# Performance work log

Measured on AMD Instinct MI355X. Metric: run time of the kernel, lower is better.

## Reference

```python
import jax, jax.numpy as jnp
import numpy as np

B, S, D = 16, 2000, 512          # batch, seq_len, input_dim
G, K = 2, 320                    # num_groups, num_vars
CV = 256                         # codevector_dim
d = CV // G                      # per-group codevector dim
TAU = 2.0                        # gumbel-softmax temperature (module default)
EPS = 1e-7


def setup_inputs() -> dict:
    key = jax.random.key(0)
    k0, k1, k2, k3, k4 = jax.random.split(key, 5)
    hidden_states = jax.random.normal(k0, (B, S, D), jnp.float32)
    mask_time_indices = jax.random.randint(k1, (B, S), 0, 2) > 0
    W = jax.random.normal(k2, (G * K, D), jnp.float32) * 0.02  # weight_proj
    b = jnp.zeros((G * K,), jnp.float32)
    codevectors = jax.random.uniform(k3, (1, G * K, d), jnp.float32)  # uniform_ init
    u = jax.random.uniform(k4, (B * S * G, K), jnp.float32, minval=1e-6, maxval=1.0 - 1e-6)
    gumbel = -jnp.log(-jnp.log(u))  # standard Gumbel(0,1) noise
    return dict(hidden_states=hidden_states, mask_time_indices=mask_time_indices,
                W=W, b=b, codevectors=codevectors, gumbel=gumbel)


def _compute_perplexity(probs, mask):
    # probs: (B*S, G, K); mask: (B, S) bool
    mask_f = mask.reshape(-1).astype(probs.dtype)[:, None, None]
    marginal = (probs * mask_f).sum(0) / mask_f.sum()          # (G, K)
    return jnp.exp(-jnp.sum(marginal * jnp.log(marginal + EPS), axis=-1)).sum()


def reference(hidden_states, mask_time_indices, W, b, codevectors, gumbel):
    # weight projection: (B, S, G*K)
    logits = jnp.einsum('bsd,vd->bsv', hidden_states, W) + b
    logits = logits.reshape(B * S * G, K)

    # hard gumbel-softmax (training path), straight-through estimator
    y_soft = jax.nn.softmax((logits + gumbel) / TAU, axis=-1)
    idx = jnp.argmax(y_soft, axis=-1)
    y_hard = jax.nn.one_hot(idx, K, dtype=y_soft.dtype)
    codevector_probs = y_hard + y_soft - jax.lax.stop_gradient(y_soft)

    # perplexity from the soft (non-gumbel, non-tempered) distribution
    soft_dist = jax.nn.softmax(logits.reshape(B * S, G, K), axis=-1)
    perplexity = _compute_perplexity(soft_dist, mask_time_indices)

    # weighted sum of codevectors per group; einsum avoids the (B*S, G*K, d) blowup
    cv = codevectors.reshape(G, K, d)
    out = jnp.einsum('ngk,gkd->ngd', codevector_probs.reshape(B * S, G, K), cv)
    out = out.reshape(B, S, G * d)  # (B, S, codevector_dim)
    return out, perplexity
```

## Files before the change

### kernel.cpp

```cpp
#include <hip/hip_runtime.h>

#define NB    16
#define NS    2000
#define ND    512
#define NG    2
#define NK    320
#define NV    640
#define NDCV  128
#define NTOK  32000
#define TAUF  2.0f
#define EPSF  1e-7f

#define TPB      16
#define NTHREADS 640
#define TIE_THR  2.5e-3f

using half8   = __attribute__((ext_vector_type(8))) _Float16;
using half4   = __attribute__((ext_vector_type(4))) _Float16;
using float4v = __attribute__((ext_vector_type(4))) float;

__device__ inline half8 cvt8hi(float4 p0, float4 p1) {
    half8 a;
    a[0] = (_Float16)p0.x; a[1] = (_Float16)p0.y;
    a[2] = (_Float16)p0.z; a[3] = (_Float16)p0.w;
    a[4] = (_Float16)p1.x; a[5] = (_Float16)p1.y;
    a[6] = (_Float16)p1.z; a[7] = (_Float16)p1.w;
    return a;
}

__device__ inline half4 cvt4hi(float4 p) {
    half4 a;
    a[0] = (_Float16)p.x; a[1] = (_Float16)p.y;
    a[2] = (_Float16)p.z; a[3] = (_Float16)p.w;
    return a;
}

__device__ inline bool beats(float za, int ka, float zb, int kb) {
    return (za > zb) || (za == zb && ka < kb);
}

__global__ void k_wsplit(const float* __restrict__ W, half8* __restrict__ W1p) {
    int t = blockIdx.x * 256 + threadIdx.x;
    if (t >= NV * (ND / 8)) return;
    int v  = t % NV;
    int kc = t / NV;
    const float* src = W + (size_t)v * ND + kc * 8;
    float4 p0 = *(const float4*)src;
    float4 p1 = *(const float4*)(src + 4);
    W1p[t] = cvt8hi(p0, p1);
}

#define AROWB 128
__global__ __launch_bounds__(1024, 4) void k_gemm(
    const float* __restrict__ hidden,
    const half8* __restrict__ W1p,
    const float* __restrict__ bvec,
    float* __restrict__ logits)
{
    __shared__ __align__(16) char Abuf[2][64 * AROWB];

    const int t    = threadIdx.x;
    const int lane = t & 63;
    const int w    = t >> 6;
    const int wn   = w & 7;
    const int wm   = w >> 3;
    const int l15  = lane & 15;
    const int l4   = lane >> 4;
    const int n0b  = blockIdx.x * 64;

    const int sm  = t >> 4;
    const int sk4 = t & 15;
    const float* hrow = hidden + (size_t)(n0b + sm) * ND + sk4 * 4;
    const int wbyte = sm * AROWB + ((((sk4 >> 1) ^ (sm & 7)) << 4) | ((sk4 & 1) << 3));

    float4v acc[2][5];
    #pragma unroll
    for (int mt = 0; mt < 2; ++mt)
        #pragma unroll
        for (int nt = 0; nt < 5; ++nt) acc[mt][nt] = (float4v)0.0f;

    {
        float4 p = *(const float4*)(hrow);
        *(half4*)(&Abuf[0][wbyte]) = cvt4hi(p);
    }
    __syncthreads();

    const half8* bbase = W1p + (size_t)l4 * NV + wn * 80 + l15;

    for (int c = 0; c < 8; ++c) {
        float4 p;
        if (c < 7) p = *(const float4*)(hrow + (c + 1) * 64);

        const char* base = Abuf[c & 1];
        #pragma unroll
        for (int ks = 0; ks < 2; ++ks) {
            half8 b[5];
            #pragma unroll
            for (int nt = 0; nt < 5; ++nt)
                b[nt] = bbase[(size_t)(c * 8 + ks * 4) * NV + nt * 16];

            const int xr = ((ks * 4 + l4) ^ (l15 & 7)) << 4;
            half8 fa[2];
            #pragma unroll
            for (int mt = 0; mt < 2; ++mt)
                fa[mt] = *(const half8*)(base + (wm * 32 + mt * 16 + l15) * AROWB + xr);

            #pragma unroll
            for (int nt = 0; nt < 5; ++nt)
                #pragma unroll
                for (int mt = 0; mt < 2; ++mt)
                    acc[mt][nt] = __builtin_amdgcn_mfma_f32_16x16x32_f16(fa[mt], b[nt], acc[mt][nt], 0, 0, 0);
        }

        if (c < 7)
            *(half4*)(&Abuf[(c + 1) & 1][wbyte]) = cvt4hi(p);
        __syncthreads();
    }

    #pragma unroll
    for (int nt = 0; nt < 5; ++nt) {
        const int col = wn * 80 + nt * 16 + l15;
        const float bb = bvec[col];
        #pragma unroll
        for (int mt = 0; mt < 2; ++mt) {
            #pragma unroll
            for (int r = 0; r < 4; ++r) {
                const int row = n0b + wm * 32 + mt * 16 + l4 * 4 + r;
                logits[(size_t)row * NV + col] = acc[mt][nt][r] + bb;
            }
        }
    }
}

#define EPI_BLOCKS  1024
#define EPI_THREADS 256
#define EPI_SLOTS   (EPI_BLOCKS * (EPI_THREADS / 16))
#define NPAIRS      (NTOK * NG)

__global__ __launch_bounds__(EPI_THREADS) void k_epi(
    const float* __restrict__ logits,
    const float* __restrict__ gumbel,
    const int*   __restrict__ mask,
    const float* __restrict__ hidden,
    const float* __restrict__ W,
    const float* __restrict__ bvec,
    const float* __restrict__ codevec,
    float* __restrict__ out,
    float* __restrict__ marginal)
{
    __shared__ float marg[NV];
    const int t     = threadIdx.x;
    const int lane  = t & 63;
    const int q     = lane >> 4;
    const int ql    = lane & 15;
    const int wslot = blockIdx.x * (EPI_THREADS / 16) + (t >> 4);
    const int g     = wslot & 1;

    for (int i = t; i < NV; i += EPI_THREADS) marg[i] = 0.f;
    __syncthreads();

    float mreg[5][4] = {};

    int pair = wslot;
    float4 cl[5], cg[5];
    {
        const float* lrow = logits + (size_t)(pair >> 1) * NV + g * NK;
        const float* grow = gumbel + (size_t)pair * NK;
        #pragma unroll
        for (int j = 0; j < 5; ++j) {
            cl[j] = *(const float4*)(lrow + 64 * j + 4 * ql);
            cg[j] = *(const float4*)(grow + 64 * j + 4 * ql);
        }
    }

    while (true) {
        const int npair = pair + EPI_SLOTS;
        const bool nvalid = npair < NPAIRS;
        float4 nl[5], ng[5];
        if (nvalid) {
            const float* lrow = logits + (size_t)(npair >> 1) * NV + g * NK;
            const float* grow = gumbel + (size_t)npair * NK;
            #pragma unroll
            for (int j = 0; j < 5; ++j) {
                nl[j] = *(const float4*)(lrow + 64 * j + 4 * ql);
                ng[j] = *(const float4*)(grow + 64 * j + 4 * ql);
            }
        }

        const int n = pair >> 1;

        float e[5][4];
        float s = 0.f;
        #pragma unroll
        for (int j = 0; j < 5; ++j) {
            e[j][0] = __expf(cl[j].x); e[j][1] = __expf(cl[j].y);
            e[j][2] = __expf(cl[j].z); e[j][3] = __expf(cl[j].w);
            s += (e[j][0] + e[j][1]) + (e[j][2] + e[j][3]);
        }
        #pragma unroll
        for (int off = 8; off > 0; off >>= 1) s += __shfl_xor(s, off, 16);
        const float pm = (mask[n] != 0) ? (1.0f / s) : 0.0f;
        #pragma unroll
        for (int j = 0; j < 5; ++j)
            #pragma unroll
            for (int c = 0; c < 4; ++c)
                mreg[j][c] = fmaf(e[j][c], pm, mreg[j][c]);

        float z[5][4];
        #pragma unroll
        for (int j = 0; j < 5; ++j) {
            z[j][0] = cl[j].x + cg[j].x;
            z[j][1] = cl[j].y + cg[j].y;
            z[j][2] = cl[j].z + cg[j].z;
            z[j][3] = cl[j].w + cg[j].w;
        }
        float z1 = -3.4e38f; int k1 = 0;
        #pragma unroll
        for (int j = 0; j < 5; ++j)
            #pragma unroll
            for (int c = 0; c < 4; ++c) {
                const int idx = 64 * j + 4 * ql + c;
                if (z[j][c] > z1) { z1 = z[j][c]; k1 = idx; }
            }
        #pragma unroll
        for (int off = 1; off < 16; off <<= 1) {
            float oz = __shfl_xor(z1, off, 16);
            int   ok = __shfl_xor(k1, off, 16);
            if (beats(oz, ok, z1, k1)) { z1 = oz; k1 = ok; }
        }

        bool flag = false;
        #pragma unroll
        for (int j = 0; j < 5; ++j)
            #pragma unroll
            for (int c = 0; c < 4; ++c) {
                const int idx = 64 * j + 4 * ql + c;
                flag |= (idx != k1) && (z[j][c] >= z1 - TIE_THR);
            }
        const unsigned long long bal = __ballot(flag);
        const unsigned int m16 = (unsigned int)((bal >> (q * 16)) & 0xFFFFull);

        int kbest = k1;
        if (m16) {
            float z2 = -3.4e38f; int k2 = 0x7fffffff;
            #pragma unroll
            for (int j = 0; j < 5; ++j)
                #pragma unroll
                for (int c = 0; c < 4; ++c) {
                    const int idx = 64 * j + 4 * ql + c;
                    const float zz = (idx == k1) ? -3.4e38f : z[j][c];
                    if (zz > z2) { z2 = zz; k2 = idx; }
                }
            #pragma unroll
            for (int off = 1; off < 16; off <<= 1) {
                float oz = __shfl_xor(z2, off, 16);
                int   ok = __shfl_xor(k2, off, 16);
                if (beats(oz, ok, z2, k2)) { z2 = oz; k2 = ok; }
            }
            if (z1 - z2 < TIE_THR) {
                const float* hr  = hidden + (size_t)n * ND;
                const float* w1r = W + ((size_t)g * NK + k1) * ND;
                const float* w2r = W + ((size_t)g * NK + k2) * ND;
                const float* grow = gumbel + (size_t)pair * NK;
                double s1 = 0.0, s2 = 0.0;
                #pragma unroll
                for (int j = 0; j < 32; ++j) {
                    const int idx = ql * 32 + j;
                    const double h = (double)hr[idx];
                    s1 += h * (double)w1r[idx];
                    s2 += h * (double)w2r[idx];
                }
                #pragma unroll
                for (int off = 8; off > 0; off >>= 1) {
                    s1 += __shfl_xor(s1, off, 16);
                    s2 += __shfl_xor(s2, off, 16);
                }
                const double zz1 = s1 + (double)bvec[g * NK + k1] + (double)grow[k1];
                const double zz2 = s2 + (double)bvec[g * NK + k2] + (double)grow[k2];
                const bool firstWins = (zz1 > zz2) || (zz1 == zz2 && k1 < k2);
                kbest = firstWins ? k1 : k2;
            }
        }

        const float4* cvrow = (const float4*)(codevec + ((size_t)g * NK + kbest) * NDCV);
        float4* dst = (float4*)(out + (size_t)n * (NG * NDCV) + g * NDCV);
        dst[ql]      = cvrow[ql];
        dst[ql + 16] = cvrow[ql + 16];

        if (!nvalid) break;
        pair = npair;
        #pragma unroll
        for (int j = 0; j < 5; ++j) { cl[j] = nl[j]; cg[j] = ng[j]; }
    }

    #pragma unroll
    for (int j = 0; j < 5; ++j)
        #pragma unroll
        for (int c = 0; c < 4; ++c)
            atomicAdd(&marg[g * NK + 64 * j + 4 * ql + c], mreg[j][c]);
    __syncthreads();
    for (int i = t; i < NV; i += EPI_THREADS) atomicAdd(&marginal[i], marg[i]);
}

__global__ __launch_bounds__(NTHREADS) void k_finalize(
    const int* __restrict__ mask,
    const float* __restrict__ marginal,
    float* __restrict__ ppl_out)
{
    __shared__ float red[16];
    const int tid  = threadIdx.x;
    const int wave = tid >> 6;
    const int lane = tid & 63;

    float cnt = 0.f;
    for (int i = tid; i < NTOK; i += NTHREADS) cnt += (mask[i] != 0) ? 1.f : 0.f;
    #pragma unroll
    for (int off = 32; off > 0; off >>= 1) cnt += __shfl_xor(cnt, off);
    if (lane == 0) red[wave] = cnt;
    __syncthreads();
    float total = 0.f;
    #pragma unroll
    for (int wv = 0; wv < 10; wv++) total += red[wv];
    __syncthreads();

    float p = marginal[tid] / total;
    float val = p * logf(p + EPSF);
    #pragma unroll
    for (int off = 32; off > 0; off >>= 1) val += __shfl_xor(val, off);
    if (lane == 0) red[wave] = val;
    __syncthreads();
    if (tid == 0) {
        float h0 = red[0] + red[1] + red[2] + red[3] + red[4];
        float h1 = red[5] + red[6] + red[7] + red[8] + red[9];
        ppl_out[0] = expf(-h0) + expf(-h1);
    }
}

__global__ void k_transpose(const float* __restrict__ W, float* __restrict__ WT) {
    int idx = blockIdx.x * 256 + threadIdx.x;
    if (idx >= ND * NV) return;
    int k = idx / NV;
    int v = idx - k * NV;
    WT[idx] = W[v * ND + k];
}

__global__ __launch_bounds__(NTHREADS) void k_main_fb(
    const float* __restrict__ hidden,
    const int*   __restrict__ mask,
    const float* __restrict__ bvec,
    const float* __restrict__ WT,
    const float* __restrict__ codevec,
    const float* __restrict__ gumbel,
    float* __restrict__ out,
    float* __restrict__ marginal)
{
    __shared__ float smem[TPB * NV];
    __shared__ float marg_lds[NV];

    const int tid = threadIdx.x;
    const int n0  = blockIdx.x * TPB;

    marg_lds[tid] = 0.0f;
    {
        const float4* src = (const float4*)(hidden + (size_t)n0 * ND);
        float4* dst = (float4*)smem;
        for (int i = tid; i < TPB * ND / 4; i += NTHREADS) dst[i] = src[i];
    }
    __syncthreads();

    const int vgroup = tid % 160;
    const int tgroup = tid / 160;
    const int v0 = vgroup * 4;
    const int t0 = tgroup * 4;

    float acc[4][4] = {};
    const float* hbase = smem + t0 * ND;

    for (int k = 0; k < ND; k += 4) {
        float wv_[4][4], h[4][4];
        #pragma unroll
        for (int i = 0; i < 4; i++) {
            float4 tw = *(const float4*)(WT + (size_t)(k + i) * NV + v0);
            wv_[i][0] = tw.x; wv_[i][1] = tw.y; wv_[i][2] = tw.z; wv_[i][3] = tw.w;
        }
        #pragma unroll
        for (int i = 0; i < 4; i++) {
            float4 th = *(const float4*)(hbase + i * ND + k);
            h[i][0] = th.x; h[i][1] = th.y; h[i][2] = th.z; h[i][3] = th.w;
        }
        #pragma unroll
        for (int kk = 0; kk < 4; kk++)
            #pragma unroll
            for (int ti = 0; ti < 4; ti++)
                #pragma unroll
                for (int vi = 0; vi < 4; vi++)
                    acc[ti][vi] = fmaf(h[ti][kk], wv_[kk][vi], acc[ti][vi]);
    }

    __syncthreads();

    #pragma unroll
    for (int ti = 0; ti < 4; ti++) {
        float4 lv;
        lv.x = acc[ti][0] + bvec[v0 + 0];
        lv.y = acc[ti][1] + bvec[v0 + 1];
        lv.z = acc[ti][2] + bvec[v0 + 2];
        lv.w = acc[ti][3] + bvec[v0 + 3];
        *(float4*)(smem + (size_t)(t0 + ti) * NV + v0) = lv;
    }
    __syncthreads();

    const int wave = tid >> 6;
    const int lane = tid & 63;
    const int g = wave & 1;
    float marg_reg[5] = {0.f, 0.f, 0.f, 0.f, 0.f};

    for (int pair = wave; pair < 2 * TPB; pair += 10) {
        const int tt = pair >> 1;
        const int n = n0 + tt;
        const float* lrow = smem + tt * NV + g * NK;

        float lv[5];
        #pragma unroll
        for (int j = 0; j < 5; j++) lv[j] = lrow[lane + 64 * j];

        float m = lv[0];
        #pragma unroll
        for (int j = 1; j < 5; j++) m = fmaxf(m, lv[j]);
        #pragma unroll
        for (int off = 32; off > 0; off >>= 1) m = fmaxf(m, __shfl_xor(m, off));

        float e[5], s = 0.f;
        #pragma unroll
        for (int j = 0; j < 5; j++) { e[j] = expf(lv[j] - m); s += e[j]; }
        #pragma unroll
        for (int off = 32; off > 0; off >>= 1) s += __shfl_xor(s, off);
        const float inv = 1.0f / s;

        if (mask[n] != 0) {
            #pragma unroll
            for (int j = 0; j < 5; j++) marg_reg[j] += e[j] * inv;
        }

        const float* grow = gumbel + ((size_t)n * NG + g) * NK;
        float zbest = -3.4e38f;
        int kbest = 0;
        #pragma unroll
        for (int j = 0; j < 5; j++) {
            float z = lv[j] + grow[lane + 64 * j];
            if (z > zbest) { zbest = z; kbest = lane + 64 * j; }
        }
        #pragma unroll
        for (int off = 32; off > 0; off >>= 1) {
            float zo = __shfl_xor(zbest, off);
            int ko = __shfl_xor(kbest, off);
            if (zo > zbest || (zo == zbest && ko < kbest)) { zbest = zo; kbest = ko; }
        }

        const float2* cvrow = (const float2*)(codevec + ((size_t)g * NK + kbest) * NDCV);
        float2* dstrow = (float2*)(out + (size_t)n * (NG * NDCV) + g * NDCV);
        dstrow[lane] = cvrow[lane];
    }

    #pragma unroll
    for (int j = 0; j < 5; j++)
        atomicAdd(&marg_lds[g * NK + lane + 64 * j], marg_reg[j]);
    __syncthreads();
    atomicAdd(&marginal[tid], marg_lds[tid]);
}

extern "C" void kernel_launch(void* const* d_in, const int* in_sizes, int n_in,
                              void* d_out, int out_size, void* d_ws, size_t ws_size,
                              hipStream_t stream) {
    const float* hidden  = (const float*)d_in[0];
    const int*   mask    = (const int*)  d_in[1];
    const float* W       = (const float*)d_in[2];
    const float* bvec    = (const float*)d_in[3];
    const float* codevec = (const float*)d_in[4];
    const float* gumbel  = (const float*)d_in[5];
    float* out = (float*)d_out;

    float* marginal = (float*)d_ws;

    const size_t off_w1     = 4096;
    const size_t off_logits = 2u * 1024u * 1024u;
    const size_t need = off_logits + (size_t)NTOK * NV * 4;

    hipMemsetAsync(marginal, 0, NV * sizeof(float), stream);

    if (ws_size >= need) {
        half8* W1p    = (half8*)((char*)d_ws + off_w1);
        float* logits = (float*)((char*)d_ws + off_logits);

        k_wsplit<<<(NV * (ND / 8) + 255) / 256, 256, 0, stream>>>(W, W1p);
        k_gemm<<<NTOK / 64, 1024, 0, stream>>>(hidden, W1p, bvec, logits);
        k_epi<<<EPI_BLOCKS, EPI_THREADS, 0, stream>>>(logits, gumbel, mask, hidden, W, bvec,
                                                      codevec, out, marginal);
    } else {
        float* WT = (float*)d_ws + 1024;
        k_transpose<<<(ND * NV + 255) / 256, 256, 0, stream>>>(W, WT);
        k_main_fb<<<NTOK / TPB, NTHREADS, 0, stream>>>(hidden, mask, bvec, WT, codevec,
                                                       gumbel, out, marginal);
    }
    k_finalize<<<1, NTHREADS, 0, stream>>>(mask, marginal, out + (size_t)NTOK * NG * NDCV);
}
```

Measured before the change: 139.6 us.

## Fuse gumbel-argmax and perplexity epilogue into GEMM, drop logits buffer

Folds the softmax/marginal and hard-argmax epilogue into the GEMM kernel, working directly on MFMA accumulators. This removes the 82MB logits write and read-back and one kernel launch. Top-2 candidates are merged across waves through LDS, and near ties are settled with an fp64 recompute. Per-block marginals now go to a workspace and are summed by a small reduce kernel instead of global atomics. The tie threshold is widened, which may send more rows down the slow path, and gumbel loads are now strided scalar reads.

Result: slower. 152.4 us (+9.1%).

```diff
diff --git a/kernel.cpp b/kernel.cpp
--- a/kernel.cpp
+++ b/kernel.cpp
@@ -13,7 +13,8 @@
 
 #define TPB      16
 #define NTHREADS 640
-#define TIE_THR  2.5e-3f
+#define TIE_THR  4.0e-3f
+#define GEMM_BLOCKS (NTOK / 64)
 
 using half8   = __attribute__((ext_vector_type(8))) _Float16;
 using half4   = __attribute__((ext_vector_type(4))) _Float16;
@@ -51,13 +52,21 @@
 }
 
 #define AROWB 128
-__global__ __launch_bounds__(1024, 4) void k_gemm(
+__global__ __launch_bounds__(1024, 4) void k_fused(
     const float* __restrict__ hidden,
     const half8* __restrict__ W1p,
     const float* __restrict__ bvec,
-    float* __restrict__ logits)
+    const float* __restrict__ gumbel,
+    const int*   __restrict__ mask,
+    const float* __restrict__ W,
+    const float* __restrict__ codevec,
+    float* __restrict__ out,
+    float* __restrict__ marg_ws)
 {
     __shared__ __align__(16) char Abuf[2][64 * AROWB];
+    __shared__ float  marg[NV];
+    __shared__ float  ssum[64 * 2];
+    __shared__ float4 top2s[64 * 2 * 4];
 
     const int t    = threadIdx.x;
     const int lane = t & 63;
@@ -66,11 +75,16 @@
     const int wm   = w >> 3;
     const int l15  = lane & 15;
     const int l4   = lane >> 4;
-    const int n0b  = blockIdx.x * 64;
+    const int n0   = blockIdx.x * 64;
+    const int g    = wn >> 2;
+    const int wn4  = wn & 3;
+
+    for (int i = t; i < NV; i += 1024) marg[i] = 0.f;
+    if (t < 128) ssum[t] = 0.f;
 
     const int sm  = t >> 4;
     const int sk4 = t & 15;
-    const float* hrow = hidden + (size_t)(n0b + sm) * ND + sk4 * 4;
+    const float* hrow = hidden + (size_t)(n0 + sm) * ND + sk4 * 4;
     const int wbyte = sm * AROWB + ((((sk4 >> 1) ^ (sm & 7)) << 4) | ((sk4 & 1) << 3));
 
     float4v acc[2][5];
@@ -117,189 +131,177 @@
         __syncthreads();
     }
 
-    #pragma unroll
-    for (int nt = 0; nt < 5; ++nt) {
-        const int col = wn * 80 + nt * 16 + l15;
-        const float bb = bvec[col];
+    {
+        float bb[5];
+        #pragma unroll
+        for (int nt = 0; nt < 5; ++nt) bb[nt] = bvec[wn * 80 + nt * 16 + l15];
+        #pragma unroll
+        for (int mt = 0; mt < 2; ++mt)
+            #pragma unroll
+            for (int nt = 0; nt < 5; ++nt)
+                #pragma unroll
+                for (int r = 0; r < 4; ++r)
+                    acc[mt][nt][r] += bb[nt];
+    }
+
+    #pragma unroll
+    for (int mt = 0; mt < 2; ++mt) {
+        #pragma unroll
+        for (int r = 0; r < 4; ++r) {
+            const int rowblk = wm * 32 + mt * 16 + l4 * 4 + r;
+            const size_t n = n0 + rowblk;
+            const float* grow = gumbel + ((size_t)n * NG + g) * NK + wn4 * 80 + l15;
+
+            float z1 = -3.4e38f, z2 = -3.4e38f;
+            int   k1 = 0x7fffffff, k2 = 0x7fffffff;
+            #pragma unroll
+            for (int nt = 0; nt < 5; ++nt) {
+                const float zz = acc[mt][nt][r] + grow[nt * 16];
+                const int  idx = wn4 * 80 + nt * 16 + l15;
+                if (beats(zz, idx, z1, k1)) { z2 = z1; k2 = k1; z1 = zz; k1 = idx; }
+                else if (beats(zz, idx, z2, k2)) { z2 = zz; k2 = idx; }
+            }
+            #pragma unroll
+            for (int off = 1; off < 16; off <<= 1) {
+                float oz1 = __shfl_xor(z1, off, 16), oz2 = __shfl_xor(z2, off, 16);
+                int   ok1 = __shfl_xor(k1, off, 16), ok2 = __shfl_xor(k2, off, 16);
+                if (beats(oz1, ok1, z1, k1)) {
+                    if (beats(z1, k1, oz2, ok2)) { z2 = z1; k2 = k1; }
+                    else { z2 = oz2; k2 = ok2; }
+                    z1 = oz1; k1 = ok1;
+                } else if (beats(oz1, ok1, z2, k2)) {
+                    z2 = oz1; k2 = ok1;
+                }
+            }
+            if (l15 == 0) {
+                float4 tp;
+                tp.x = z1; tp.y = z2;
+                tp.z = __int_as_float(k1); tp.w = __int_as_float(k2);
+                top2s[(rowblk * 2 + g) * 4 + wn4] = tp;
+            }
+        }
+    }
+
+    #pragma unroll
+    for (int mt = 0; mt < 2; ++mt)
+        #pragma unroll
+        for (int nt = 0; nt < 5; ++nt)
+            #pragma unroll
+            for (int r = 0; r < 4; ++r)
+                acc[mt][nt][r] = __expf(acc[mt][nt][r]);
+
+    #pragma unroll
+    for (int mt = 0; mt < 2; ++mt) {
+        #pragma unroll
+        for (int r = 0; r < 4; ++r) {
+            const int rowblk = wm * 32 + mt * 16 + l4 * 4 + r;
+            float s5 = ((acc[mt][0][r] + acc[mt][1][r]) + (acc[mt][2][r] + acc[mt][3][r])) + acc[mt][4][r];
+            #pragma unroll
+            for (int off = 1; off < 16; off <<= 1) s5 += __shfl_xor(s5, off, 16);
+            if (l15 == 0) atomicAdd(&ssum[rowblk * 2 + g], s5);
+        }
+    }
+
+    __syncthreads();
+
+    {
+        float mreg[5] = {0.f, 0.f, 0.f, 0.f, 0.f};
         #pragma unroll
         for (int mt = 0; mt < 2; ++mt) {
             #pragma unroll
             for (int r = 0; r < 4; ++r) {
-                const int row = n0b + wm * 32 + mt * 16 + l4 * 4 + r;
-                logits[(size_t)row * NV + col] = acc[mt][nt][r] + bb;
-            }
-        }
-    }
-}
-
-#define EPI_BLOCKS  1024
-#define EPI_THREADS 256
-#define EPI_SLOTS   (EPI_BLOCKS * (EPI_THREADS / 16))
-#define NPAIRS      (NTOK * NG)
-
-__global__ __launch_bounds__(EPI_THREADS) void k_epi(
-    const float* __restrict__ logits,
-    const float* __restrict__ gumbel,
-    const int*   __restrict__ mask,
-    const float* __restrict__ hidden,
-    const float* __restrict__ W,
-    const float* __restrict__ bvec,
-    const float* __restrict__ codevec,
-    float* __restrict__ out,
-    float* __restrict__ marginal)
+                const int rowblk = wm * 32 + mt * 16 + l4 * 4 + r;
+                const size_t n = n0 + rowblk;
+                if (mask[n] != 0) {
+                    const float pm = 1.0f / ssum[rowblk * 2 + g];
+                    #pragma unroll
+                    for (int nt = 0; nt < 5; ++nt)
+                        mreg[nt] = fmaf(acc[mt][nt][r], pm, mreg[nt]);
+                }
+            }
+        }
+        #pragma unroll
+        for (int nt = 0; nt < 5; ++nt)
+            atomicAdd(&marg[wn * 80 + nt * 16 + l15], mreg[nt]);
+    }
+
+    for (int i = 0; i < 8; ++i) {
+        const int task   = w * 8 + i;
+        const int rowblk = task >> 1;
+        const int gg     = task & 1;
+        const size_t n   = n0 + rowblk;
+
+        const float4* tb = &top2s[(rowblk * 2 + gg) * 4];
+        float4 tp = tb[0];
+        float z1 = tp.x, z2 = tp.y;
+        int   k1 = __float_as_int(tp.z), k2 = __float_as_int(tp.w);
+        #pragma unroll
+        for (int j = 1; j < 4; ++j) {
+            tp = tb[j];
+            const float cz1 = tp.x, cz2 = tp.y;
+            const int   ck1 = __float_as_int(tp.z), ck2 = __float_as_int(tp.w);
+            if (beats(cz1, ck1, z1, k1)) {
+                if (beats(z1, k1, cz2, ck2)) { z2 = z1; k2 = k1; }
+                else { z2 = cz2; k2 = ck2; }
+                z1 = cz1; k1 = ck1;
+            } else if (beats(cz1, ck1, z2, k2)) {
+                z2 = cz1; k2 = ck1;
+            }
+        }
+
+        int kbest = k1;
+        if (z1 - z2 < TIE_THR) {
+            const float* hr  = hidden + n * ND;
+            const float* w1r = W + ((size_t)gg * NK + k1) * ND;
+            const float* w2r = W + ((size_t)gg * NK + k2) * ND;
+            double s1 = 0.0, s2 = 0.0;
+            #pragma unroll
+            for (int j = 0; j < 8; ++j) {
+                const int idx = lane * 8 + j;
+                const double h = (double)hr[idx];
+                s1 += h * (double)w1r[idx];
+                s2 += h * (double)w2r[idx];
+            }
+            #pragma unroll
+            for (int off = 1; off < 64; off <<= 1) {
+                s1 += __shfl_xor(s1, off);
+                s2 += __shfl_xor(s2, off);
+            }
+            const float* growf = gumbel + ((size_t)n * NG + gg) * NK;
+            const double zz1 = s1 + (double)bvec[gg * NK + k1] + (double)growf[k1];
+            const double zz2 = s2 + (double)bvec[gg * NK + k2] + (double)growf[k2];
+            kbest = ((zz1 > zz2) || (zz1 == zz2 && k1 < k2)) ? k1 : k2;
+        }
+
+        const float2* cvrow = (const float2*)(codevec + ((size_t)gg * NK + kbest) * NDCV);
+        float2* dst = (float2*)(out + n * (NG * NDCV) + gg * NDCV);
+        dst[lane] = cvrow[lane];
+    }
+
+    __syncthreads();
+    float* dstm = marg_ws + (size_t)blockIdx.x * NV;
+    for (int i = t; i < NV; i += 1024) dstm[i] = marg[i];
+}
+
+__global__ __launch_bounds__(256) void k_reduce(
+    const float* __restrict__ marg_ws, float* __restrict__ marginal)
 {
-    __shared__ float marg[NV];
-    const int t     = threadIdx.x;
-    const int lane  = t & 63;
-    const int q     = lane >> 4;
-    const int ql    = lane & 15;
-    const int wslot = blockIdx.x * (EPI_THREADS / 16) + (t >> 4);
-    const int g     = wslot & 1;
-
-    for (int i = t; i < NV; i += EPI_THREADS) marg[i] = 0.f;
-    __syncthreads();
-
-    float mreg[5][4] = {};
-
-    int pair = wslot;
-    float4 cl[5], cg[5];
-    {
-        const float* lrow = logits + (size_t)(pair >> 1) * NV + g * NK;
-        const float* grow = gumbel + (size_t)pair * NK;
-        #pragma unroll
-        for (int j = 0; j < 5; ++j) {
-            cl[j] = *(const float4*)(lrow + 64 * j + 4 * ql);
-            cg[j] = *(const float4*)(grow + 64 * j + 4 * ql);
-        }
-    }
-
-    while (true) {
-        const int npair = pair + EPI_SLOTS;
-        const bool nvalid = npair < NPAIRS;
-        float4 nl[5], ng[5];
-        if (nvalid) {
-            const float* lrow = logits + (size_t)(npair >> 1) * NV + g * NK;
-            const float* grow = gumbel + (size_t)npair * NK;
-            #pragma unroll
-            for (int j = 0; j < 5; ++j) {
-                nl[j] = *(const float4*)(lrow + 64 * j + 4 * ql);
-                ng[j] = *(const float4*)(grow + 64 * j + 4 * ql);
-            }
-        }
-
-        const int n = pair >> 1;
-
-        float e[5][4];
-        float s = 0.f;
-        #pragma unroll
-        for (int j = 0; j < 5; ++j) {
-            e[j][0] = __expf(cl[j].x); e[j][1] = __expf(cl[j].y);
-            e[j][2] = __expf(cl[j].z); e[j][3] = __expf(cl[j].w);
-            s += (e[j][0] + e[j][1]) + (e[j][2] + e[j][3]);
-        }
-        #pragma unroll
-        for (int off = 8; off > 0; off >>= 1) s += __shfl_xor(s, off, 16);
-        const float pm = (mask[n] != 0) ? (1.0f / s) : 0.0f;
-        #pragma unroll
-        for (int j = 0; j < 5; ++j)
-            #pragma unroll
-            for (int c = 0; c < 4; ++c)
-                mreg[j][c] = fmaf(e[j][c], pm, mreg[j][c]);
-
-        float z[5][4];
-        #pragma unroll
-        for (int j = 0; j < 5; ++j) {
-            z[j][0] = cl[j].x + cg[j].x;
-            z[j][1] = cl[j].y + cg[j].y;
-            z[j][2] = cl[j].z + cg[j].z;
-            z[j][3] = cl[j].w + cg[j].w;
-        }
-        float z1 = -3.4e38f; int k1 = 0;
-        #pragma unroll
-        for (int j = 0; j < 5; ++j)
-            #pragma unroll
-            for (int c = 0; c < 4; ++c) {
-                const int idx = 64 * j + 4 * ql + c;
-                if (z[j][c] > z1) { z1 = z[j][c]; k1 = idx; }
-            }
-        #pragma unroll
-        for (int off = 1; off < 16; off <<= 1) {
-            float oz = __shfl_xor(z1, off, 16);
-            int   ok = __shfl_xor(k1, off, 16);
-            if (beats(oz, ok, z1, k1)) { z1 = oz; k1 = ok; }
-        }
-
-        bool flag = false;
-        #pragma unroll
-        for (int j = 0; j < 5; ++j)
-            #pragma unroll
-            for (int c = 0; c < 4; ++c) {
-                const int idx = 64 * j + 4 * ql + c;
-                flag |= (idx != k1) && (z[j][c] >= z1 - TIE_THR);
-            }
-        const unsigned long long bal = __ballot(flag);
-        const unsigned int m16 = (unsigned int)((bal >> (q * 16)) & 0xFFFFull);
-
-        int kbest = k1;
-        if (m16) {
-            float z2 = -3.4e38f; int k2 = 0x7fffffff;
-            #pragma unroll
-            for (int j = 0; j < 5; ++j)
-                #pragma unroll
-                for (int c = 0; c < 4; ++c) {
-                    const int idx = 64 * j + 4 * ql + c;
-                    const float zz = (idx == k1) ? -3.4e38f : z[j][c];
-                    if (zz > z2) { z2 = zz; k2 = idx; }
-                }
-            #pragma unroll
-            for (int off = 1; off < 16; off <<= 1) {
-                float oz = __shfl_xor(z2, off, 16);
-                int   ok = __shfl_xor(k2, off, 16);
-                if (beats(oz, ok, z2, k2)) { z2 = oz; k2 = ok; }
-            }
-            if (z1 - z2 < TIE_THR) {
-                const float* hr  = hidden + (size_t)n * ND;
-                const float* w1r = W + ((size_t)g * NK + k1) * ND;
-                const float* w2r = W + ((size_t)g * NK + k2) * ND;
-                const float* grow = gumbel + (size_t)pair * NK;
-                double s1 = 0.0, s2 = 0.0;
-                #pragma unroll
-                for (int j = 0; j < 32; ++j) {
-                    const int idx = ql * 32 + j;
-                    const double h = (double)hr[idx];
-                    s1 += h * (double)w1r[idx];
-                    s2 += h * (double)w2r[idx];
-                }
-                #pragma unroll
-                for (int off = 8; off > 0; off >>= 1) {
-                    s1 += __shfl_xor(s1, off, 16);
-                    s2 += __shfl_xor(s2, off, 16);
-                }
-                const double zz1 = s1 + (double)bvec[g * NK + k1] + (double)grow[k1];
-                const double zz2 = s2 + (double)bvec[g * NK + k2] + (double)grow[k2];
-                const bool firstWins = (zz1 > zz2) || (zz1 == zz2 && k1 < k2);
-                kbest = firstWins ? k1 : k2;
-            }
-        }
-
-        const float4* cvrow = (const float4*)(codevec + ((size_t)g * NK + kbest) * NDCV);
-        float4* dst = (float4*)(out + (size_t)n * (NG * NDCV) + g * NDCV);
-        dst[ql]      = cvrow[ql];
-        dst[ql + 16] = cvrow[ql + 16];
-
-        if (!nvalid) break;
-        pair = npair;
-        #pragma unroll
-        for (int j = 0; j < 5; ++j) { cl[j] = nl[j]; cg[j] = ng[j]; }
-    }
-
-    #pragma unroll
-    for (int j = 0; j < 5; ++j)
-        #pragma unroll
-        for (int c = 0; c < 4; ++c)
-            atomicAdd(&marg[g * NK + 64 * j + 4 * ql + c], mreg[j][c]);
-    __syncthreads();
-    for (int i = t; i < NV; i += EPI_THREADS) atomicAdd(&marginal[i], marg[i]);
+    __shared__ float red[8][32];
+    const int v  = blockIdx.x * 32 + (threadIdx.x & 31);
+    const int ch = threadIdx.x >> 5;
+
+    float s = 0.f;
+    for (int i = ch; i < GEMM_BLOCKS; i += 8)
+        s += marg_ws[(size_t)i * NV + v];
+
+    red[ch][threadIdx.x & 31] = s;
+    __syncthreads();
+    if (ch == 0) {
+        float tot = s;
+        #pragma unroll
+        for (int c = 1; c < 8; ++c) tot += red[c][threadIdx.x & 31];
+        marginal[v] = tot;
+    }
 }
 
 __global__ __launch_bounds__(NTHREADS) void k_finalize(
@@ -483,19 +485,19 @@
     float* marginal = (float*)d_ws;
 
     const size_t off_w1     = 4096;
-    const size_t off_logits = 2u * 1024u * 1024u;
-    const size_t need = off_logits + (size_t)NTOK * NV * 4;
+    const size_t off_margws = 1u * 1024u * 1024u;
+    const size_t need = off_margws + (size_t)GEMM_BLOCKS * NV * 4;
 
     hipMemsetAsync(marginal, 0, NV * sizeof(float), stream);
 
     if (ws_size >= need) {
-        half8* W1p    = (half8*)((char*)d_ws + off_w1);
-        float* logits = (float*)((char*)d_ws + off_logits);
+        half8* W1p     = (half8*)((char*)d_ws + off_w1);
+        float* marg_ws = (float*)((char*)d_ws + off_margws);
 
         k_wsplit<<<(NV * (ND / 8) + 255) / 256, 256, 0, stream>>>(W, W1p);
-        k_gemm<<<NTOK / 64, 1024, 0, stream>>>(hidden, W1p, bvec, logits);
-        k_epi<<<EPI_BLOCKS, EPI_THREADS, 0, stream>>>(logits, gumbel, mask, hidden, W, bvec,
-                                                      codevec, out, marginal);
+        k_fused<<<GEMM_BLOCKS, 1024, 0, stream>>>(hidden, W1p, bvec, gumbel, mask,
+                                                  W, codevec, out, marg_ws);
+        k_reduce<<<NV / 32, 256, 0, stream>>>(marg_ws, marginal);
     } else {
         float* WT = (float*)d_ws + 1024;
         k_transpose<<<(ND * NV + 255) / 256, 256, 0, stream>>>(W, WT);
```
